# Kernel optimization log

Measured on AMD Instinct MI355X. Metric: run time of the kernel, lower is better.

## Reference

```python
import jax, jax.numpy as jnp
import numpy as np

N_NODES = 100000
N_EDGES = 1600000
D_IN = 128
D_HID = 128
D_OUT = 64


def setup_inputs() -> dict:
    key = jax.random.key(0)
    ks = jax.random.split(key, 8)
    x = jax.random.normal(ks[0], (N_NODES, D_IN), dtype=jnp.float32)
    edge_index = jax.random.randint(ks[1], (2, N_EDGES), 0, N_NODES, dtype=jnp.int64)
    s = 1.0 / np.sqrt(D_IN)
    W1l = jax.random.uniform(ks[2], (D_IN, D_HID), minval=-s, maxval=s, dtype=jnp.float32)
    W1r = jax.random.uniform(ks[3], (D_IN, D_HID), minval=-s, maxval=s, dtype=jnp.float32)
    b1 = jnp.zeros((D_HID,), dtype=jnp.float32)
    s2 = 1.0 / np.sqrt(D_HID)
    W2l = jax.random.uniform(ks[4], (D_HID, D_OUT), minval=-s2, maxval=s2, dtype=jnp.float32)
    W2r = jax.random.uniform(ks[5], (D_HID, D_OUT), minval=-s2, maxval=s2, dtype=jnp.float32)
    b2 = jnp.zeros((D_OUT,), dtype=jnp.float32)
    return {"x": x, "edge_index": edge_index, "drpt": 0,
            "W1l": W1l, "W1r": W1r, "b1": b1,
            "W2l": W2l, "W2r": W2r, "b2": b2}


def _mean_aggregate(x, src, dst, n_nodes):
    # gather source features along edges, scatter-mean to destinations
    gathered = x[src]                                   # [E, d]
    summed = jax.ops.segment_sum(gathered, dst, num_segments=n_nodes)  # [N, d]
    deg = jax.ops.segment_sum(jnp.ones((src.shape[0],), x.dtype), dst,
                              num_segments=n_nodes)     # [N]
    return summed / jnp.maximum(deg, 1.0)[:, None]


def _sage_conv(x, src, dst, Wl, Wr, b):
    # PyG SAGEConv (mean): out = agg @ Wl + b + x @ Wr
    agg = _mean_aggregate(x, src, dst, x.shape[0])
    return agg @ Wl + b + x @ Wr


def reference(x, edge_index, drpt, W1l, W1r, b1, W2l, W2r, b2):
    src, dst = edge_index[0], edge_index[1]
    h = _sage_conv(x, src, dst, W1l, W1r, b1)
    h = jax.nn.relu(h)
    # dropout is identity at inference (training=False)
    out = _sage_conv(h, src, dst, W2l, W2r, b2)
    return out
```

## Files before the change

kernel.cpp:

```cpp
#include <hip/hip_runtime.h>
#include <hip/hip_bf16.h>


#define N_NODES 100000
#define NGRP 6250
#define NBKT 391
#define ECHUNK 8192
#define BCAP 12288
#define NXB 12500
#define NWB 192

typedef __attribute__((ext_vector_type(8))) short short8v;
typedef __attribute__((ext_vector_type(4))) float f32x4;
typedef __attribute__((ext_vector_type(2))) uint u32x2;

__device__ inline ushort bf16_rne(float f) {
    union { float f; uint u; } c; c.f = f;
    uint u = c.u;
    return (ushort)((u + 0x7FFFu + ((u >> 16) & 1u)) >> 16);
}
__device__ inline float bf16_f(ushort h) {
    union { uint u; float f; } c; c.u = (uint)h << 16;
    return c.f;
}
__device__ inline unsigned char fp8_enc(float f) {
    union { float f; uint u; } c; c.f = f;
    uint u = c.u;
    uint s = (u >> 24) & 0x80u;
    uint a = u & 0x7FFFFFFFu;
    uint code;
    if (a >= 0x3C800000u) {
        uint r = a + 0x7FFFFu + ((a >> 20) & 1u);
        int e = (int)(r >> 23) - 120;
        uint mm = (r >> 20) & 7u;
        code = ((uint)e << 3) | mm;
        if (code > 0x7Eu) code = 0x7Eu;
    } else {
        code = (uint)(__uint_as_float(a) * 512.0f + 0.5f);
    }
    return (unsigned char)(s | code);
}

__device__ inline void gl_lds16(const void* g, void* l) {
    __builtin_amdgcn_global_load_lds(
        (const __attribute__((address_space(1))) uint*)g,
        (__attribute__((address_space(3))) uint*)l, 16, 0, 0);
}
__device__ inline uint lds_off(const void* p) {
    return (uint)(size_t)(const __attribute__((address_space(3))) char*)p;
}

__global__ __launch_bounds__(256) void k_prep(const float* __restrict__ x,
                                              const float* __restrict__ W1l,
                                              const float* __restrict__ W1r,
                                              const float* __restrict__ W2l,
                                              const float* __restrict__ W2r,
                                              const int* __restrict__ dst, int E,
                                              ushort* __restrict__ xh,
                                              unsigned char* __restrict__ xf8,
                                              ushort* __restrict__ BT1h,
                                              ushort* __restrict__ BT1l,
                                              ushort* __restrict__ BT2h,
                                              ushort* __restrict__ BT2l,
                                              int* __restrict__ bhist) {
    __shared__ int hsh[NBKT];
    const int b = blockIdx.x;
    if (b < NXB) {
        int i = (b * 256 + threadIdx.x) * 4;
        float4 v = *(const float4*)&x[i];
        ushort4 hh;
        hh.x = bf16_rne(v.x); hh.y = bf16_rne(v.y);
        hh.z = bf16_rne(v.z); hh.w = bf16_rne(v.w);
        *(ushort4*)&xh[i] = hh;
        uint f8 = (uint)fp8_enc(v.x) | ((uint)fp8_enc(v.y) << 8) |
                  ((uint)fp8_enc(v.z) << 16) | ((uint)fp8_enc(v.w) << 24);
        *(uint*)&xf8[i] = f8;
    } else if (b < NXB + NWB) {
        int id = (b - NXB) * 256 + threadIdx.x;
        if (id < 32768) {
            int n = id >> 8, k = id & 255;
            float v = (k < 128) ? W1l[k * 128 + n] : W1r[(k - 128) * 128 + n];
            ushort h = bf16_rne(v);
            BT1h[id] = h;
            BT1l[id] = bf16_rne(v - bf16_f(h));
        } else {
            int i = id - 32768;
            int n = i >> 7, k = i & 127;
            float v = (n < 64) ? W2l[k * 64 + n] : W2r[k * 64 + (n - 64)];
            ushort h = bf16_rne(v);
            BT2h[i] = h;
            BT2l[i] = bf16_rne(v - bf16_f(h));
        }
    } else {
        int bb = b - NXB - NWB;
        for (int i = threadIdx.x; i < NBKT; i += 256) hsh[i] = 0;
        __syncthreads();
        int b0 = bb * ECHUNK;
        for (int i = threadIdx.x; i < ECHUNK; i += 256) {
            int e = b0 + i;
            if (e < E) atomicAdd(&hsh[dst[e] >> 8], 1);
        }
        __syncthreads();
        for (int i = threadIdx.x; i < NBKT; i += 256)
            if (hsh[i]) atomicAdd(&bhist[i], hsh[i]);
    }
}

__global__ __launch_bounds__(512) void kA2_scan(const int* __restrict__ bhist,
                                                int* __restrict__ boff,
                                                int* __restrict__ bcur) {
    __shared__ int s[512];
    int t = threadIdx.x;
    s[t] = (t < NBKT) ? bhist[t] : 0;
    __syncthreads();
    for (int d = 1; d < 512; d <<= 1) {
        int v = (t >= d) ? s[t - d] : 0;
        __syncthreads();
        s[t] += v;
        __syncthreads();
    }
    if (t <= NBKT) {
        int e = (t == 0) ? 0 : s[t - 1];
        boff[t] = e;
        if (t < NBKT) bcur[t] = e;
    }
}

__global__ __launch_bounds__(256) void kA3_scatter(const int* __restrict__ src,
                                                   const int* __restrict__ dst,
                                                   int* __restrict__ bcur,
                                                   int* __restrict__ pairs, int E) {
    __shared__ int hist[NBKT];
    __shared__ int base[NBKT];
    __shared__ ushort rank[ECHUNK];
    for (int i = threadIdx.x; i < NBKT; i += 256) hist[i] = 0;
    __syncthreads();
    int b0 = blockIdx.x * ECHUNK;
    for (int i = threadIdx.x; i < ECHUNK; i += 256) {
        int e = b0 + i;
        if (e < E) rank[i] = (ushort)atomicAdd(&hist[dst[e] >> 8], 1);
    }
    __syncthreads();
    for (int i = threadIdx.x; i < NBKT; i += 256) {
        int c = hist[i];
        base[i] = c ? atomicAdd(&bcur[i], c) : 0;
    }
    __syncthreads();
    for (int i = threadIdx.x; i < ECHUNK; i += 256) {
        int e = b0 + i;
        if (e < E) {
            int d = dst[e];
            pairs[base[d >> 8] + rank[i]] = src[e] | ((d & 255) << 17);
        }
    }
}

__global__ __launch_bounds__(256) void kB_build(const int* __restrict__ pairs,
                                                const int* __restrict__ boff,
                                                int* __restrict__ csr,
                                                unsigned char* __restrict__ ldst,
                                                int* __restrict__ offsets,
                                                float* __restrict__ invdeg,
                                                int N, int E) {
    __shared__ int cntk[256];
    __shared__ int sck[256];
    __shared__ int cur[256];
    __shared__ int cntn[256];
    __shared__ int stage[BCAP];
    const int b = blockIdx.x;
    const int gbase = boff[b], gcount = boff[b + 1] - gbase;
    const int n0 = b << 8;
    const int t = threadIdx.x;

    cntk[t] = 0; cntn[t] = 0;
    __syncthreads();
    for (int i = t; i < gcount; i += 256) {
        int p = pairs[gbase + i];
        int dlow = (p >> 17) & 255;
        int key = (dlow & 0xF0) | ((p & 0x1FFFF) >> 13);
        atomicAdd(&cntk[key], 1);
        atomicAdd(&cntn[dlow], 1);
    }
    __syncthreads();
    sck[t] = cntk[t];
    __syncthreads();
    for (int d = 1; d < 256; d <<= 1) {
        int v = (t >= d) ? sck[t - d] : 0;
        __syncthreads();
        sck[t] += v;
        __syncthreads();
    }
    cur[t] = sck[t] - cntk[t];
    int node = n0 + t;
    if (node < N) {
        int gk = t & 0xF0;
        offsets[node] = gbase + sck[gk] - cntk[gk];
        invdeg[node] = 1.0f / fmaxf((float)cntn[t], 1.0f);
    }
    if (b == NBKT - 1 && t == 0) offsets[N] = E;
    __syncthreads();

    if (gcount <= BCAP) {
        for (int i = t; i < gcount; i += 256) {
            int p = pairs[gbase + i];
            int key = ((p >> 17) & 0xF0) | ((p & 0x1FFFF) >> 13);
            int pos = atomicAdd(&cur[key], 1);
            stage[pos] = p;
        }
        __syncthreads();
        for (int i = t; i < gcount; i += 256) {
            int p = stage[i];
            csr[gbase + i] = p & 0x1FFFF;
            ldst[gbase + i] = (unsigned char)((p >> 17) & 15);
        }
    } else {
        for (int i = t; i < gcount; i += 256) {
            int p = pairs[gbase + i];
            int key = ((p >> 17) & 0xF0) | ((p & 0x1FFFF) >> 13);
            int pos = atomicAdd(&cur[key], 1);
            csr[gbase + pos] = p & 0x1FFFF;
            ldst[gbase + pos] = (unsigned char)((p >> 17) & 15);
        }
    }
}

__global__ __launch_bounds__(64, 8) void k_agg1(const unsigned char* __restrict__ xf8,
                                                const int* __restrict__ csr,
                                                const unsigned char* __restrict__ ldst,
                                                const int* __restrict__ off,
                                                const float* __restrict__ invdeg,
                                                ushort* __restrict__ ah, int E) {
    __shared__ __align__(1024) char stg[4096];
    const int lane = threadIdx.x;
    const int g = blockIdx.x;
    const int gbase = off[g * 16], gend = off[g * 16 + 16];
    const int cnt = gend - gbase;
    const int m = lane & 15;
    const int e_meta = lane & 31;
    const int Emax = E - 1;
    const int esrc = lane >> 3;
    const int koff = ((lane & 7) ^ (esrc & 7)) << 4;

    f32x4 acc[8] = {};
    const int nch = (cnt + 31) >> 5;

    int pe = gbase + e_meta;
    int se = csr[(pe < Emax) ? pe : Emax];
    int lb = (pe < gend) ? (int)ldst[pe] : 255;

    const uint e7 = (lane >> 1) & 7;
    const uint bbase = lds_off(stg) + (uint)((lane >> 1) * 128 + (lane & 1) * 8);

    for (int ch = 0; ch < nch; ++ch) {
        #pragma unroll
        for (int c = 0; c < 4; ++c) {
            int rs = __shfl(se, c * 8 + esrc);
            gl_lds16((const char*)xf8 + (size_t)rs * 128 + koff, stg + c * 1024);
        }

        int p = gbase + (ch + 1) * 32 + e_meta;
        se = csr[(p < Emax) ? p : Emax];
        int lbn = (p < gend) ? (int)ldst[p] : 255;

        asm volatile("s_waitcnt vmcnt(0)" ::: "memory");
        __builtin_amdgcn_sched_barrier(0);

        unsigned long long av = 0ull;
        #pragma unroll
        for (int j = 0; j < 8; ++j) {
            int k = (lane >> 4) * 8 + j;
            int b = __shfl(lb, k);
            av |= (b == m) ? (0x38ull << (8 * j)) : 0ull;
        }

        #pragma unroll
        for (int th = 0; th < 2; ++th) {
            u32x2 tb[4];
            #pragma unroll
            for (int t4 = 0; t4 < 4; ++t4) {
                uint t = (uint)(th * 4 + t4);
                uint a1 = bbase + ((t ^ e7) << 4);
                asm volatile("ds_read_b64_tr_b8 %0, %1" : "=v"(tb[t4]) : "v"(a1));
            }
            asm volatile("s_waitcnt lgkmcnt(0)" ::: "memory");
            __builtin_amdgcn_sched_barrier(0);
            #pragma unroll
            for (int t4 = 0; t4 < 4; ++t4) {
                unsigned long long bv = ((unsigned long long)tb[t4].y << 32) | tb[t4].x;
                acc[th * 4 + t4] = __builtin_amdgcn_mfma_f32_16x16x32_fp8_fp8(
                    (long long)av, (long long)bv, acc[th * 4 + t4], 0, 0, 0);
            }
            __builtin_amdgcn_sched_barrier(0);
        }
        lb = lbn;
    }

    float idv[4];
    #pragma unroll
    for (int i = 0; i < 4; ++i) idv[i] = invdeg[g * 16 + (lane >> 4) * 4 + i];
    #pragma unroll
    for (int t = 0; t < 8; ++t) {
        #pragma unroll
        for (int i = 0; i < 4; ++i) {
            int node = g * 16 + (lane >> 4) * 4 + i;
            ah[(size_t)node * 128 + t * 16 + m] = bf16_rne(acc[t][i] * idv[i]);
        }
    }
}

__global__ __launch_bounds__(64, 8) void k_agg2(const ushort* __restrict__ hWl,
                                                const float* __restrict__ hWr,
                                                const int* __restrict__ csr,
                                                const unsigned char* __restrict__ ldst,
                                                const int* __restrict__ off,
                                                const float* __restrict__ invdeg,
                                                const float* __restrict__ b2,
                                                float* __restrict__ out, int E) {
    __shared__ __align__(1024) char stg[4096];
    const int lane = threadIdx.x;
    const int g = blockIdx.x;
    const int gbase = off[g * 16], gend = off[g * 16 + 16];
    const int cnt = gend - gbase;
    const int m = lane & 15;
    const int e_meta = lane & 31;
    const int Emax = E - 1;
    const int esrc = lane >> 3;
    const int koff = ((lane & 7) ^ ((esrc & 3) << 1)) << 4;

    f32x4 acc[4] = {};
    const int nch = (cnt + 31) >> 5;

    int pe = gbase + e_meta;
    int se = csr[(pe < Emax) ? pe : Emax];
    int lb = (pe < gend) ? (int)ldst[pe] : 255;

    const uint he = ((lane >> 1) & 1) ^ (((lane >> 2) & 3) << 1);
    const uint bbase = lds_off(stg) +
        (uint)(((lane >> 4) * 8 + ((lane >> 2) & 3)) * 128 + (lane & 1) * 8);

    for (int ch = 0; ch < nch; ++ch) {
        #pragma unroll
        for (int c = 0; c < 4; ++c) {
            int rs = __shfl(se, c * 8 + esrc);
            gl_lds16((const char*)hWl + (size_t)rs * 128 + koff, stg + c * 1024);
        }

        int p = gbase + (ch + 1) * 32 + e_meta;
        se = csr[(p < Emax) ? p : Emax];
        int lbn = (p < gend) ? (int)ldst[p] : 255;

        asm volatile("s_waitcnt vmcnt(0)" ::: "memory");
        __builtin_amdgcn_sched_barrier(0);

        uint au[4];
        #pragma unroll
        for (int jp = 0; jp < 4; ++jp) {
            int k0 = (lane >> 4) * 8 + jp * 2;
            int b0 = __shfl(lb, k0);
            int b1 = __shfl(lb, k0 + 1);
            au[jp] = ((b0 == m) ? 0x3F80u : 0u) | (((b1 == m) ? 0x3F80u : 0u) << 16);
        }
        union { uint u[4]; short8v v; } A_;
        A_.u[0] = au[0]; A_.u[1] = au[1]; A_.u[2] = au[2]; A_.u[3] = au[3];

        #pragma unroll
        for (int th = 0; th < 2; ++th) {
            u32x2 t1[2], t2[2];
            #pragma unroll
            for (int tt = 0; tt < 2; ++tt) {
                uint t = (uint)(th * 2 + tt);
                uint seg = (2u * t) ^ he;
                uint a1 = bbase + (seg << 4);
                uint a2 = a1 + 512;
                asm volatile("ds_read_b64_tr_b16 %0, %1" : "=v"(t1[tt]) : "v"(a1));
                asm volatile("ds_read_b64_tr_b16 %0, %1" : "=v"(t2[tt]) : "v"(a2));
            }
            asm volatile("s_waitcnt lgkmcnt(0)" ::: "memory");
            __builtin_amdgcn_sched_barrier(0);
            #pragma unroll
            for (int tt = 0; tt < 2; ++tt) {
                union { uint u[4]; short8v v; } B_;
                B_.u[0] = t1[tt].x; B_.u[1] = t1[tt].y;
                B_.u[2] = t2[tt].x; B_.u[3] = t2[tt].y;
                acc[th * 2 + tt] = __builtin_amdgcn_mfma_f32_16x16x32_bf16(
                    A_.v, B_.v, acc[th * 2 + tt], 0, 0, 0);
            }
            __builtin_amdgcn_sched_barrier(0);
        }
        lb = lbn;
    }

    float idv[4];
    #pragma unroll
    for (int i = 0; i < 4; ++i) idv[i] = invdeg[g * 16 + (lane >> 4) * 4 + i];
    #pragma unroll
    for (int t = 0; t < 4; ++t) {
        #pragma unroll
        for (int i = 0; i < 4; ++i) {
            int node = g * 16 + (lane >> 4) * 4 + i;
            size_t idx = (size_t)node * 64 + t * 16 + m;
            out[idx] = acc[t][i] * idv[i] + hWr[idx] + b2[t * 16 + m];
        }
    }
}

__global__ __launch_bounds__(256) void k_mfma12(
    const ushort* __restrict__ Agg, const ushort* __restrict__ X,
    const ushort* __restrict__ B1h, const ushort* __restrict__ B1l,
    const ushort* __restrict__ B2h, const ushort* __restrict__ B2l,
    const float* __restrict__ b1,
    ushort* __restrict__ hWl, float* __restrict__ hWr, int M) {
    __shared__ ushort Ah[128 * 40], Bh[128 * 40], Bl[128 * 40];
    __shared__ ushort hT[4 * 128 * 40];

    const int tid = threadIdx.x;
    const int wid = tid >> 6, lane = tid & 63;
    const int wm = wid >> 1, wn = wid & 1;
    const int m0 = blockIdx.x * 128;
    const int rl = lane & 15, kof = (lane >> 4) * 8;
    const int rq = lane >> 4;

    const int r0 = tid >> 2, r1 = (tid + 256) >> 2;
    const int cq = tid & 3;
    int g0 = m0 + r0; if (g0 >= M) g0 = M - 1;
    int g1 = m0 + r1; if (g1 >= M) g1 = M - 1;
    const int ldso0 = r0 * 40 + cq * 8;
    const int ldso1 = r1 * 40 + cq * 8;

    short8v pA0, pA1, pB0, pB1, pL0, pL1;
    {
        int gk = cq * 8;
        pA0 = *(const short8v*)&Agg[(size_t)g0 * 128 + gk];
        pA1 = *(const short8v*)&Agg[(size_t)g1 * 128 + gk];
        pB0 = *(const short8v*)&B1h[r0 * 256 + gk];
        pB1 = *(const short8v*)&B1h[r1 * 256 + gk];
        pL0 = *(const short8v*)&B1l[r0 * 256 + gk];
        pL1 = *(const short8v*)&B1l[r1 * 256 + gk];
    }
    f32x4 acc[4][4] = {};
    for (int kc = 0; kc < 8; ++kc) {
        *(short8v*)&Ah[ldso0] = pA0; *(short8v*)&Ah[ldso1] = pA1;
        *(short8v*)&Bh[ldso0] = pB0; *(short8v*)&Bh[ldso1] = pB1;
        *(short8v*)&Bl[ldso0] = pL0; *(short8v*)&Bl[ldso1] = pL1;
        __syncthreads();

        if (kc < 7) {
            int gk = (kc + 1) * 32 + cq * 8;
            const ushort* s0 = (gk >= 128) ? &X[(size_t)g0 * 128 + gk - 128]
                                           : &Agg[(size_t)g0 * 128 + gk];
            const ushort* s1 = (gk >= 128) ? &X[(size_t)g1 * 128 + gk - 128]
                                           : &Agg[(size_t)g1 * 128 + gk];
            pA0 = *(const short8v*)s0;
            pA1 = *(const short8v*)s1;
            pB0 = *(const short8v*)&B1h[r0 * 256 + gk];
            pB1 = *(const short8v*)&B1h[r1 * 256 + gk];
            pL0 = *(const short8v*)&B1l[r0 * 256 + gk];
            pL1 = *(const short8v*)&B1l[r1 * 256 + gk];
        }

        short8v a_h[4], b_h[4], b_l[4];
        #pragma unroll
        for (int f = 0; f < 4; ++f) {
            int ra = wm * 64 + f * 16 + rl;
            int rb = wn * 64 + f * 16 + rl;
            a_h[f] = *(const short8v*)&Ah[ra * 40 + kof];
            b_h[f] = *(const short8v*)&Bh[rb * 40 + kof];
            b_l[f] = *(const short8v*)&Bl[rb * 40 + kof];
        }
        #pragma unroll
        for (int mf = 0; mf < 4; ++mf)
            #pragma unroll
            for (int nf = 0; nf < 4; ++nf) {
                acc[mf][nf] = __builtin_amdgcn_mfma_f32_16x16x32_bf16(a_h[mf], b_h[nf], acc[mf][nf], 0, 0, 0);
                acc[mf][nf] = __builtin_amdgcn_mfma_f32_16x16x32_bf16(a_h[mf], b_l[nf], acc[mf][nf], 0, 0, 0);
            }
        __syncthreads();
    }

    short8v qB0, qB1, qL0, qL1;
    {
        int gk = cq * 8;
        qB0 = *(const short8v*)&B2h[r0 * 128 + gk];
        qB1 = *(const short8v*)&B2h[r1 * 128 + gk];
        qL0 = *(const short8v*)&B2l[r0 * 128 + gk];
        qL1 = *(const short8v*)&B2l[r1 * 128 + gk];
    }

    #pragma unroll
    for (int mf = 0; mf < 4; ++mf)
        #pragma unroll
        for (int nf = 0; nf < 4; ++nf) {
            int col = wn * 64 + nf * 16 + rl;
            float bv = b1[col];
            #pragma unroll
            for (int i = 0; i < 4; ++i) {
                int rloc = wm * 64 + mf * 16 + rq * 4 + i;
                float v = fmaxf(acc[mf][nf][i] + bv, 0.0f);
                hT[((col >> 5) * 128 + rloc) * 40 + (col & 31)] = bf16_rne(v);
            }
        }
    __syncthreads();

    f32x4 acc2[4][4] = {};
    for (int kc = 0; kc < 4; ++kc) {
        *(short8v*)&Bh[ldso0] = qB0; *(short8v*)&Bh[ldso1] = qB1;
        *(short8v*)&Bl[ldso0] = qL0; *(short8v*)&Bl[ldso1] = qL1;
        __syncthreads();

        if (kc < 3) {
            int gk = (kc + 1) * 32 + cq * 8;
            qB0 = *(const short8v*)&B2h[r0 * 128 + gk];
            qB1 = *(const short8v*)&B2h[r1 * 128 + gk];
            qL0 = *(const short8v*)&B2l[r0 * 128 + gk];
            qL1 = *(const short8v*)&B2l[r1 * 128 + gk];
        }

        short8v a_h[4], b_h[4], b_l[4];
        #pragma unroll
        for (int f = 0; f < 4; ++f) {
            int ra = wm * 64 + f * 16 + rl;
            int rb = wn * 64 + f * 16 + rl;
            a_h[f] = *(const short8v*)&hT[(kc * 128 + ra) * 40 + kof];
            b_h[f] = *(const short8v*)&Bh[rb * 40 + kof];
            b_l[f] = *(const short8v*)&Bl[rb * 40 + kof];
        }
        #pragma unroll
        for (int mf = 0; mf < 4; ++mf)
            #pragma unroll
            for (int nf = 0; nf < 4; ++nf) {
                acc2[mf][nf] = __builtin_amdgcn_mfma_f32_16x16x32_bf16(a_h[mf], b_h[nf], acc2[mf][nf], 0, 0, 0);
                acc2[mf][nf] = __builtin_amdgcn_mfma_f32_16x16x32_bf16(a_h[mf], b_l[nf], acc2[mf][nf], 0, 0, 0);
            }
        __syncthreads();
    }

    #pragma unroll
    for (int mf = 0; mf < 4; ++mf)
        #pragma unroll
        for (int nf = 0; nf < 4; ++nf) {
            int col = wn * 64 + nf * 16 + rl;
            #pragma unroll
            for (int i = 0; i < 4; ++i) {
                int row = m0 + wm * 64 + mf * 16 + rq * 4 + i;
                if (row < M) {
                    float v = acc2[mf][nf][i];
                    if (col < 64) hWl[(size_t)row * 64 + col] = bf16_rne(v);
                    else          hWr[(size_t)row * 64 + col - 64] = v;
                }
            }
        }
}

extern "C" void kernel_launch(void* const* d_in, const int* in_sizes, int n_in,
                              void* d_out, int out_size, void* d_ws, size_t ws_size,
                              hipStream_t stream) {
    const float* x   = (const float*)d_in[0];
    const int*   ei  = (const int*)d_in[1];
    const float* W1l = (const float*)d_in[3];
    const float* W1r = (const float*)d_in[4];
    const float* b1  = (const float*)d_in[5];
    const float* W2l = (const float*)d_in[6];
    const float* W2r = (const float*)d_in[7];
    const float* b2  = (const float*)d_in[8];
    float* out = (float*)d_out;

    const int N = N_NODES;
    const int E = in_sizes[1] / 2;
    const int* src = ei;
    const int* dst = ei + E;
    const int NEB = (E + ECHUNK - 1) / ECHUNK;

    char* ws = (char*)d_ws;
    int*           bhist   = (int*)   (ws + 0);
    int*           boff    = (int*)   (ws + 4096);
    int*           bcur    = (int*)   (ws + 8192);
    int*           offsets = (int*)   (ws + 12288);
    float*         invdeg  = (float*) (ws + 417792);
    int*           csr     = (int*)   (ws + 819200);
    unsigned char* ldst    = (unsigned char*)(ws + 7220224);
    unsigned char* x_f8    = (unsigned char*)(ws + 8821760);
    ushort*        x_hi    = (ushort*)(ws + 21622784);
    ushort*        agg_hi  = (ushort*)(ws + 47223808);
    float*         hWr     = (float*) (ws + 98425856);
    ushort*        BT1h    = (ushort*)(ws + 124026880);
    ushort*        BT1l    = (ushort*)(ws + 124092416);
    ushort*        BT2h    = (ushort*)(ws + 124157952);
    ushort*        BT2l    = (ushort*)(ws + 124190720);
    int*           pairs   = (int*)   (ws + 98425856);
    ushort*        hWl     = (ushort*)(ws + 72824832);

    hipMemsetAsync(bhist, 0, NBKT * 4, stream);

    k_prep<<<NXB + NWB + NEB, 256, 0, stream>>>(x, W1l, W1r, W2l, W2r, dst, E,
                                                x_hi, x_f8, BT1h, BT1l, BT2h, BT2l, bhist);
    kA2_scan<<<1, 512, 0, stream>>>(bhist, boff, bcur);
    kA3_scatter<<<NEB, 256, 0, stream>>>(src, dst, bcur, pairs, E);
    kB_build<<<NBKT, 256, 0, stream>>>(pairs, boff, csr, ldst, offsets, invdeg, N, E);

    k_agg1<<<NGRP, 64, 0, stream>>>(x_f8, csr, ldst, offsets, invdeg, agg_hi, E);

    const int MB = (N + 127) / 128;
    k_mfma12<<<MB, 256, 0, stream>>>(agg_hi, x_hi, BT1h, BT1l, BT2h, BT2l,
                                     b1, hWl, hWr, N);

    k_agg2<<<NGRP, 64, 0, stream>>>(hWl, hWr, csr, ldst, offsets, invdeg, b2, out, E);
}
```

Measured before the change: 173.6 us.

## Load MFMA fragments directly from global memory, bypassing LDS staging in fused GEMM

```diff
diff --git a/kernel.cpp b/kernel.cpp
--- a/kernel.cpp
+++ b/kernel.cpp
@@ -404,13 +404,12 @@
     }
 }
 
-__global__ __launch_bounds__(256) void k_mfma12(
+__global__ __launch_bounds__(256, 2) void k_mfma12(
     const ushort* __restrict__ Agg, const ushort* __restrict__ X,
     const ushort* __restrict__ B1h, const ushort* __restrict__ B1l,
     const ushort* __restrict__ B2h, const ushort* __restrict__ B2l,
     const float* __restrict__ b1,
     ushort* __restrict__ hWl, float* __restrict__ hWr, int M) {
-    __shared__ ushort Ah[128 * 40], Bh[128 * 40], Bl[128 * 40];
     __shared__ ushort hT[4 * 128 * 40];
 
     const int tid = threadIdx.x;
@@ -420,70 +419,55 @@
     const int rl = lane & 15, kof = (lane >> 4) * 8;
     const int rq = lane >> 4;
 
-    const int r0 = tid >> 2, r1 = (tid + 256) >> 2;
-    const int cq = tid & 3;
-    int g0 = m0 + r0; if (g0 >= M) g0 = M - 1;
-    int g1 = m0 + r1; if (g1 >= M) g1 = M - 1;
-    const int ldso0 = r0 * 40 + cq * 8;
-    const int ldso1 = r1 * 40 + cq * 8;
-
-    short8v pA0, pA1, pB0, pB1, pL0, pL1;
-    {
-        int gk = cq * 8;
-        pA0 = *(const short8v*)&Agg[(size_t)g0 * 128 + gk];
-        pA1 = *(const short8v*)&Agg[(size_t)g1 * 128 + gk];
-        pB0 = *(const short8v*)&B1h[r0 * 256 + gk];
-        pB1 = *(const short8v*)&B1h[r1 * 256 + gk];
-        pL0 = *(const short8v*)&B1l[r0 * 256 + gk];
-        pL1 = *(const short8v*)&B1l[r1 * 256 + gk];
+    int raG[4], rbW[4];
+    #pragma unroll
+    for (int f = 0; f < 4; ++f) {
+        int r = m0 + wm * 64 + f * 16 + rl;
+        raG[f] = (r < M) ? r : (M - 1);
+        rbW[f] = wn * 64 + f * 16 + rl;
+    }
+
+    short8v aC[4], bhC[4], blC[4];
+    #pragma unroll
+    for (int f = 0; f < 4; ++f) {
+        aC[f]  = *(const short8v*)&Agg[(size_t)raG[f] * 128 + kof];
+        bhC[f] = *(const short8v*)&B1h[rbW[f] * 256 + kof];
+        blC[f] = *(const short8v*)&B1l[rbW[f] * 256 + kof];
     }
     f32x4 acc[4][4] = {};
+    #pragma unroll
     for (int kc = 0; kc < 8; ++kc) {
-        *(short8v*)&Ah[ldso0] = pA0; *(short8v*)&Ah[ldso1] = pA1;
-        *(short8v*)&Bh[ldso0] = pB0; *(short8v*)&Bh[ldso1] = pB1;
-        *(short8v*)&Bl[ldso0] = pL0; *(short8v*)&Bl[ldso1] = pL1;
-        __syncthreads();
-
+        short8v aN[4], bhN[4], blN[4];
         if (kc < 7) {
-            int gk = (kc + 1) * 32 + cq * 8;
-            const ushort* s0 = (gk >= 128) ? &X[(size_t)g0 * 128 + gk - 128]
-                                           : &Agg[(size_t)g0 * 128 + gk];
-            const ushort* s1 = (gk >= 128) ? &X[(size_t)g1 * 128 + gk - 128]
-                                           : &Agg[(size_t)g1 * 128 + gk];
-            pA0 = *(const short8v*)s0;
-            pA1 = *(const short8v*)s1;
-            pB0 = *(const short8v*)&B1h[r0 * 256 + gk];
-            pB1 = *(const short8v*)&B1h[r1 * 256 + gk];
-            pL0 = *(const short8v*)&B1l[r0 * 256 + gk];
-            pL1 = *(const short8v*)&B1l[r1 * 256 + gk];
-        }
-
-        short8v a_h[4], b_h[4], b_l[4];
-        #pragma unroll
-        for (int f = 0; f < 4; ++f) {
-            int ra = wm * 64 + f * 16 + rl;
-            int rb = wn * 64 + f * 16 + rl;
-            a_h[f] = *(const short8v*)&Ah[ra * 40 + kof];
-            b_h[f] = *(const short8v*)&Bh[rb * 40 + kof];
-            b_l[f] = *(const short8v*)&Bl[rb * 40 + kof];
+            #pragma unroll
+            for (int f = 0; f < 4; ++f) {
+                int gk = (kc + 1) * 32 + kof;
+                aN[f]  = (kc + 1 >= 4)
+                       ? *(const short8v*)&X[(size_t)raG[f] * 128 + gk - 128]
+                       : *(const short8v*)&Agg[(size_t)raG[f] * 128 + gk];
+                bhN[f] = *(const short8v*)&B1h[rbW[f] * 256 + gk];
+                blN[f] = *(const short8v*)&B1l[rbW[f] * 256 + gk];
+            }
+        } else {
+            #pragma unroll
+            for (int f = 0; f < 4; ++f) { aN[f] = aC[f]; bhN[f] = bhC[f]; blN[f] = blC[f]; }
         }
         #pragma unroll
         for (int mf = 0; mf < 4; ++mf)
             #pragma unroll
             for (int nf = 0; nf < 4; ++nf) {
-                acc[mf][nf] = __builtin_amdgcn_mfma_f32_16x16x32_bf16(a_h[mf], b_h[nf], acc[mf][nf], 0, 0, 0);
-                acc[mf][nf] = __builtin_amdgcn_mfma_f32_16x16x32_bf16(a_h[mf], b_l[nf], acc[mf][nf], 0, 0, 0);
-            }
-        __syncthreads();
-    }
-
-    short8v qB0, qB1, qL0, qL1;
-    {
-        int gk = cq * 8;
-        qB0 = *(const short8v*)&B2h[r0 * 128 + gk];
-        qB1 = *(const short8v*)&B2h[r1 * 128 + gk];
-        qL0 = *(const short8v*)&B2l[r0 * 128 + gk];
-        qL1 = *(const short8v*)&B2l[r1 * 128 + gk];
+                acc[mf][nf] = __builtin_amdgcn_mfma_f32_16x16x32_bf16(aC[mf], bhC[nf], acc[mf][nf], 0, 0, 0);
+                acc[mf][nf] = __builtin_amdgcn_mfma_f32_16x16x32_bf16(aC[mf], blC[nf], acc[mf][nf], 0, 0, 0);
+            }
+        #pragma unroll
+        for (int f = 0; f < 4; ++f) { aC[f] = aN[f]; bhC[f] = bhN[f]; blC[f] = blN[f]; }
+    }
+
+    short8v qh[4], ql[4];
+    #pragma unroll
+    for (int f = 0; f < 4; ++f) {
+        qh[f] = *(const short8v*)&B2h[rbW[f] * 128 + kof];
+        ql[f] = *(const short8v*)&B2l[rbW[f] * 128 + kof];
     }
 
     #pragma unroll
@@ -502,36 +486,35 @@
     __syncthreads();
 
     f32x4 acc2[4][4] = {};
+    #pragma unroll
     for (int kc = 0; kc < 4; ++kc) {
-        *(short8v*)&Bh[ldso0] = qB0; *(short8v*)&Bh[ldso1] = qB1;
-        *(short8v*)&Bl[ldso0] = qL0; *(short8v*)&Bl[ldso1] = qL1;
-        __syncthreads();
-
+        short8v qhN[4], qlN[4];
         if (kc < 3) {
-            int gk = (kc + 1) * 32 + cq * 8;
-            qB0 = *(const short8v*)&B2h[r0 * 128 + gk];
-            qB1 = *(const short8v*)&B2h[r1 * 128 + gk];
-            qL0 = *(const short8v*)&B2l[r0 * 128 + gk];
-            qL1 = *(const short8v*)&B2l[r1 * 128 + gk];
-        }
-
-        short8v a_h[4], b_h[4], b_l[4];
+            #pragma unroll
+            for (int f = 0; f < 4; ++f) {
+                int gk = (kc + 1) * 32 + kof;
+                qhN[f] = *(const short8v*)&B2h[rbW[f] * 128 + gk];
+                qlN[f] = *(const short8v*)&B2l[rbW[f] * 128 + gk];
+            }
+        } else {
+            #pragma unroll
+            for (int f = 0; f < 4; ++f) { qhN[f] = qh[f]; qlN[f] = ql[f]; }
+        }
+        short8v a2[4];
         #pragma unroll
         for (int f = 0; f < 4; ++f) {
             int ra = wm * 64 + f * 16 + rl;
-            int rb = wn * 64 + f * 16 + rl;
-            a_h[f] = *(const short8v*)&hT[(kc * 128 + ra) * 40 + kof];
-            b_h[f] = *(const short8v*)&Bh[rb * 40 + kof];
-            b_l[f] = *(const short8v*)&Bl[rb * 40 + kof];
+            a2[f] = *(const short8v*)&hT[(kc * 128 + ra) * 40 + kof];
         }
         #pragma unroll
         for (int mf = 0; mf < 4; ++mf)
             #pragma unroll
             for (int nf = 0; nf < 4; ++nf) {
-                acc2[mf][nf] = __builtin_amdgcn_mfma_f32_16x16x32_bf16(a_h[mf], b_h[nf], acc2[mf][nf], 0, 0, 0);
-                acc2[mf][nf] = __builtin_amdgcn_mfma_f32_16x16x32_bf16(a_h[mf], b_l[nf], acc2[mf][nf], 0, 0, 0);
-            }
-        __syncthreads();
+                acc2[mf][nf] = __builtin_amdgcn_mfma_f32_16x16x32_bf16(a2[mf], qh[nf], acc2[mf][nf], 0, 0, 0);
+                acc2[mf][nf] = __builtin_amdgcn_mfma_f32_16x16x32_bf16(a2[mf], ql[nf], acc2[mf][nf], 0, 0, 0);
+            }
+        #pragma unroll
+        for (int f = 0; f < 4; ++f) { qh[f] = qhN[f]; ql[f] = qlN[f]; }
     }
 
     #pragma unroll
```

Result: slower. 200.8 us (+15.7%).

## Alias LDS buffers and use k-major unpadded layout to raise MFMA kernel occupancy

Applied to the files above, without the earlier changes.

```diff
diff --git a/kernel.cpp b/kernel.cpp
--- a/kernel.cpp
+++ b/kernel.cpp
@@ -404,28 +404,32 @@
     }
 }
 
-__global__ __launch_bounds__(256) void k_mfma12(
+__global__ __launch_bounds__(256, 3) void k_mfma12(
     const ushort* __restrict__ Agg, const ushort* __restrict__ X,
     const ushort* __restrict__ B1h, const ushort* __restrict__ B1l,
     const ushort* __restrict__ B2h, const ushort* __restrict__ B2l,
     const float* __restrict__ b1,
     ushort* __restrict__ hWl, float* __restrict__ hWr, int M) {
-    __shared__ ushort Ah[128 * 40], Bh[128 * 40], Bl[128 * 40];
-    __shared__ ushort hT[4 * 128 * 40];
+    __shared__ ushort SM[24576];
+    ushort* Bh = SM;
+    ushort* Bl = SM + 4096;
+    ushort* Ah = SM + 8192;
+    ushort* hT = SM + 8192;
 
     const int tid = threadIdx.x;
     const int wid = tid >> 6, lane = tid & 63;
     const int wm = wid >> 1, wn = wid & 1;
     const int m0 = blockIdx.x * 128;
-    const int rl = lane & 15, kof = (lane >> 4) * 8;
+    const int rl = lane & 15, kq = lane >> 4;
+    const int kof = kq * 8;
     const int rq = lane >> 4;
 
     const int r0 = tid >> 2, r1 = (tid + 256) >> 2;
     const int cq = tid & 3;
     int g0 = m0 + r0; if (g0 >= M) g0 = M - 1;
     int g1 = m0 + r1; if (g1 >= M) g1 = M - 1;
-    const int ldso0 = r0 * 40 + cq * 8;
-    const int ldso1 = r1 * 40 + cq * 8;
+    const int ldso0 = cq * 1024 + r0 * 8;
+    const int ldso1 = cq * 1024 + r1 * 8;
 
     short8v pA0, pA1, pB0, pB1, pL0, pL1;
     {
@@ -463,9 +467,9 @@
         for (int f = 0; f < 4; ++f) {
             int ra = wm * 64 + f * 16 + rl;
             int rb = wn * 64 + f * 16 + rl;
-            a_h[f] = *(const short8v*)&Ah[ra * 40 + kof];
-            b_h[f] = *(const short8v*)&Bh[rb * 40 + kof];
-            b_l[f] = *(const short8v*)&Bl[rb * 40 + kof];
+            a_h[f] = *(const short8v*)&Ah[kq * 1024 + ra * 8];
+            b_h[f] = *(const short8v*)&Bh[kq * 1024 + rb * 8];
+            b_l[f] = *(const short8v*)&Bl[kq * 1024 + rb * 8];
         }
         #pragma unroll
         for (int mf = 0; mf < 4; ++mf)
@@ -492,11 +496,12 @@
         for (int nf = 0; nf < 4; ++nf) {
             int col = wn * 64 + nf * 16 + rl;
             float bv = b1[col];
+            int cbase = (col >> 5) * 4096 + ((col & 31) >> 3) * 1024 + (col & 7);
             #pragma unroll
             for (int i = 0; i < 4; ++i) {
                 int rloc = wm * 64 + mf * 16 + rq * 4 + i;
                 float v = fmaxf(acc[mf][nf][i] + bv, 0.0f);
-                hT[((col >> 5) * 128 + rloc) * 40 + (col & 31)] = bf16_rne(v);
+                hT[cbase + rloc * 8] = bf16_rne(v);
             }
         }
     __syncthreads();
@@ -520,9 +525,9 @@
         for (int f = 0; f < 4; ++f) {
             int ra = wm * 64 + f * 16 + rl;
             int rb = wn * 64 + f * 16 + rl;
-            a_h[f] = *(const short8v*)&hT[(kc * 128 + ra) * 40 + kof];
-            b_h[f] = *(const short8v*)&Bh[rb * 40 + kof];
-            b_l[f] = *(const short8v*)&Bl[rb * 40 + kof];
+            a_h[f] = *(const short8v*)&hT[kc * 4096 + kq * 1024 + ra * 8];
+            b_h[f] = *(const short8v*)&Bh[kq * 1024 + rb * 8];
+            b_l[f] = *(const short8v*)&Bl[kq * 1024 + rb * 8];
         }
         #pragma unroll
         for (int mf = 0; mf < 4; ++mf)
```

Result: no change. 172.7 us (-0.5%).
